# Kernel optimization log

Measured on AMD Instinct MI355X. Metric: run time of the kernel, lower is better.

## Reference

```python
import jax, jax.numpy as jnp
from jax import lax
import numpy as np

B, C, H, W = 4, 256, 64, 64
CQK = C // 8  # 32


def conv3x3(x, w, b):
    # x: [B,C_in,H,W], w: [C_out,C_in,3,3], b: [C_out]
    y = lax.conv_general_dilated(x, w, window_strides=(1, 1), padding='SAME',
                                 dimension_numbers=('NCHW', 'OIHW', 'NCHW'))
    return y + b[None, :, None, None]


def setup_inputs() -> dict:
    key = jax.random.key(0)
    ks = jax.random.split(key, 8)
    scale = 0.02
    return {
        'x': jax.random.normal(ks[0], (B, C, H, W), dtype=jnp.float32),
        'wq': jax.random.normal(ks[1], (CQK, C, 3, 3), dtype=jnp.float32) * scale,
        'bq': jax.random.normal(ks[2], (CQK,), dtype=jnp.float32) * scale,
        'wk': jax.random.normal(ks[3], (CQK, C, 3, 3), dtype=jnp.float32) * scale,
        'bk': jax.random.normal(ks[4], (CQK,), dtype=jnp.float32) * scale,
        'wv': jax.random.normal(ks[5], (C, C, 3, 3), dtype=jnp.float32) * scale,
        'bv': jax.random.normal(ks[6], (C,), dtype=jnp.float32) * scale,
        'gamma': jax.random.normal(ks[7], (1,), dtype=jnp.float32) * scale,
    }


def reference(x, wq, bq, wk, bk, wv, bv, gamma):
    b, c, h, w = x.shape
    n = h * w
    # Q: [B, N, C//8]  (permute(0,2,1) of the flattened conv output)
    q = conv3x3(x, wq, bq).reshape(b, -1, n).transpose(0, 2, 1)
    # K: [B, C//8, N]
    k = conv3x3(x, wk, bk).reshape(b, -1, n)
    # s: [B, N_q, N_k]
    s = jnp.einsum('bqd,bdk->bqk', q, k)
    # NOTE: original uses Softmax(dim=-2), i.e. over the QUERY axis
    attn_T = jax.nn.softmax(s, axis=-2)
    # V: [B, C, N]
    v = conv3x3(x, wv, bv).reshape(b, c, n)
    # o = bmm(V, attn_T): [B, C, N]
    o = jnp.einsum('bcq,bqk->bck', v, attn_T).reshape(b, c, h, w)
    return x + gamma * o
```

## Files before the change

### kernel.cpp

```cpp
#include <hip/hip_runtime.h>
#include <cstddef>

#define N_PIX 4096
#define HW 64
#define LOG2E 1.4426950408889634f
#define SHIFT2 28.8539008177793f

typedef __attribute__((ext_vector_type(8))) short bf16x8;
typedef __attribute__((ext_vector_type(4))) float f32x4;
typedef unsigned int u32;

static __device__ __forceinline__ unsigned short f2bf(float f) {
    union { float f; unsigned u; } v; v.f = f;
    unsigned r = v.u + 0x7fffu + ((v.u >> 16) & 1u);
    return (unsigned short)(r >> 16);
}
static __device__ __forceinline__ float bf2f(unsigned short s) {
    union { unsigned u; float f; } v; v.u = (unsigned)s << 16;
    return v.f;
}
static __device__ __forceinline__ unsigned pack_bf16_trunc(float lo, float hi) {
    union { float f; unsigned u; } a, b; a.f = hi; b.f = lo;
    return __builtin_amdgcn_perm(a.u, b.u, 0x07060302u);
}
static __device__ __forceinline__ void gll16(const void* g, void* l) {
    __builtin_amdgcn_global_load_lds(
        (const __attribute__((address_space(1))) u32*)g,
        (__attribute__((address_space(3))) u32*)l, 16, 0, 0);
}

__global__ __launch_bounds__(256) void prep_kernel(
    const float* __restrict__ x, unsigned short* __restrict__ xbf,
    const float* __restrict__ wq, const float* __restrict__ wk,
    const float* __restrict__ wv, unsigned short* __restrict__ wAll,
    unsigned short* __restrict__ zp)
{
    const int tid = threadIdx.x;
    if (blockIdx.z < 4) {
        __shared__ unsigned short Ts[64][72];
        const int px0 = blockIdx.x * 64, ci0 = blockIdx.y * 64, b = blockIdx.z;
        const float* xb = x + ((size_t)b * 256 + ci0) * N_PIX;

#pragma unroll
        for (int r = 0; r < 4; ++r) {
            int c = r * 16 + (tid >> 4);
            int p4 = (tid & 15) * 4;
            float4 v = *(const float4*)&xb[(size_t)c * N_PIX + px0 + p4];
            Ts[c][p4 + 0] = f2bf(v.x);
            Ts[c][p4 + 1] = f2bf(v.y);
            Ts[c][p4 + 2] = f2bf(v.z);
            Ts[c][p4 + 3] = f2bf(v.w);
        }
        __syncthreads();
#pragma unroll
        for (int r = 0; r < 2; ++r) {
            int id = tid * 2 + r;
            int p = id >> 3, c8 = (id & 7) * 8;
            ushort4 lo, hi;
            lo.x = Ts[c8 + 0][p]; lo.y = Ts[c8 + 1][p];
            lo.z = Ts[c8 + 2][p]; lo.w = Ts[c8 + 3][p];
            hi.x = Ts[c8 + 4][p]; hi.y = Ts[c8 + 5][p];
            hi.z = Ts[c8 + 6][p]; hi.w = Ts[c8 + 7][p];
            size_t off = ((size_t)b * N_PIX + px0 + p) * 256 + ci0 + c8;
            *(ushort4*)&xbf[off]     = lo;
            *(ushort4*)&xbf[off + 4] = hi;
        }
    } else {
        const int f = blockIdx.y * 64 + blockIdx.x;
#pragma unroll
        for (int base = 0; base < 2; ++base) {
            int gid = base * 65536 + f * 256 + tid;
            if (gid < 256) zp[gid] = 0;
            if (gid >= 72 * 320 * 4) continue;
            int part = gid & 3;
            int m = (gid >> 2) % 320;
            int kb = gid / 1280;
            int t = kb >> 3;
            int ci0 = (kb & 7) * 32 + part * 8;
            const float* src; int co; float sc = 1.f;
            if (m < 256)      { src = wv; co = m; }
            else if (m < 288) { src = wq; co = m - 256; sc = LOG2E; }
            else              { src = wk; co = m - 288; }
            ushort4 lo, hi;
            lo.x = f2bf(sc * src[((size_t)co * 256 + ci0 + 0) * 9 + t]);
            lo.y = f2bf(sc * src[((size_t)co * 256 + ci0 + 1) * 9 + t]);
            lo.z = f2bf(sc * src[((size_t)co * 256 + ci0 + 2) * 9 + t]);
            lo.w = f2bf(sc * src[((size_t)co * 256 + ci0 + 3) * 9 + t]);
            hi.x = f2bf(sc * src[((size_t)co * 256 + ci0 + 4) * 9 + t]);
            hi.y = f2bf(sc * src[((size_t)co * 256 + ci0 + 5) * 9 + t]);
            hi.z = f2bf(sc * src[((size_t)co * 256 + ci0 + 6) * 9 + t]);
            hi.w = f2bf(sc * src[((size_t)co * 256 + ci0 + 7) * 9 + t]);
            size_t off = ((size_t)kb * 320 + m) * 32 + part * 8;
            *(ushort4*)&wAll[off]     = lo;
            *(ushort4*)&wAll[off + 4] = hi;
        }
    }
}

__global__ __launch_bounds__(256, 2) void conv_gemm_v9(
    const unsigned short* __restrict__ xbf, const unsigned short* __restrict__ wAll,
    const float* __restrict__ bq, const float* __restrict__ bk,
    const float* __restrict__ bv, const unsigned short* __restrict__ zpage,
    unsigned short* __restrict__ vbf, unsigned short* __restrict__ qt,
    unsigned short* __restrict__ kt)
{
    __shared__ unsigned short Bl[3 * 7168];

    const int tid = threadIdx.x;
    const int w = tid >> 6, lane = tid & 63, quad = lane >> 4, l15 = lane & 15;
    const int y = blockIdx.x, rh = blockIdx.y, b = blockIdx.z;
    const int rg = w >> 1;
    const int pxh = w & 1;

    const unsigned short* xb = xbf + (size_t)b * N_PIX * 256;
    const unsigned short* aSrc = wAll + (size_t)rh * 160 * 32;

    auto stage = [&](int kb, int buf) {
        const int t_ = kb >> 3;
        const int ty = t_ / 3;
        const int dy = ty - 1, dx = t_ - ty * 3 - 1;
        const int gy = y + dy;
        const bool rowOK = ((unsigned)gy < 64u);
        const int ci0 = (kb & 7) * 32;
        const unsigned short* aS = aSrc + (size_t)kb * 10240;
        unsigned short* tile = &Bl[buf * 7168];
#pragma unroll
        for (int r = 0; r < 4; ++r) {
            const int c = r * 4 + w;
            if (r == 3 && w >= 2) continue;
            if (c < 10) {
                int o = c * 1024 + lane * 16;
                int u = o ^ (((o >> 7) & 7) << 4);
                gll16(aS + (u >> 1), tile + c * 512);
            } else {
                int o = (c - 10) * 1024 + lane * 16;
                int u = o ^ (((o >> 7) & 7) << 4);
                int px = u >> 6, k16 = (u >> 4) & 3;
                int gx = px + dx;
                const unsigned short* src =
                    (rowOK && (unsigned)gx < 64u)
                        ? xb + ((size_t)(gy * 64 + gx) * 256 + ci0 + k16 * 8)
                        : zpage;
                gll16(src, tile + 5120 + (c - 10) * 512);
            }
        }
    };

    f32x4 acc[5][2];
#pragma unroll
    for (int cb = 0; cb < 5; ++cb)
#pragma unroll
        for (int jb = 0; jb < 2; ++jb) acc[cb][jb] = (f32x4){0.f, 0.f, 0.f, 0.f};

    stage(0, 0);
    stage(1, 1);
    if (w < 2) asm volatile("s_waitcnt vmcnt(4)" ::: "memory");
    else       asm volatile("s_waitcnt vmcnt(3)" ::: "memory");
    __builtin_amdgcn_s_barrier();
    __builtin_amdgcn_sched_barrier(0);

#pragma unroll
    for (int kb = 0; kb < 72; ++kb) {
        const int buf = kb % 3;
        const int pb  = (kb + 2) % 3;
        const bool more2 = (kb + 2 < 72);
        const bool more1 = (kb + 1 < 72);
        if (more2) stage(kb + 2, pb);

        const int bb = buf * 7168;
        bf16x8 af[5], bfr[2];
#pragma unroll
        for (int cb = 0; cb < 5; ++cb) {
            int sr = rg * 80 + cb * 16 + l15;
            int u = sr * 64 + quad * 16;
            u ^= ((u >> 7) & 7) << 4;
            af[cb] = *(const bf16x8*)&Bl[bb + (u >> 1)];
        }
#pragma unroll
        for (int jb = 0; jb < 2; ++jb) {
            int px = pxh * 32 + jb * 16 + l15;
            int u = px * 64 + quad * 16;
            u ^= ((u >> 7) & 7) << 4;
            bfr[jb] = *(const bf16x8*)&Bl[bb + 5120 + (u >> 1)];
        }
        __builtin_amdgcn_s_setprio(1);
#pragma unroll
        for (int cb = 0; cb < 5; ++cb)
#pragma unroll
            for (int jb = 0; jb < 2; ++jb)
                acc[cb][jb] = __builtin_amdgcn_mfma_f32_16x16x32_bf16(
                    af[cb], bfr[jb], acc[cb][jb], 0, 0, 0);
        __builtin_amdgcn_s_setprio(0);

        if (more2) {
            if (w < 2) asm volatile("s_waitcnt vmcnt(4)" ::: "memory");
            else       asm volatile("s_waitcnt vmcnt(3)" ::: "memory");
        } else if (more1) {
            asm volatile("s_waitcnt vmcnt(0)" ::: "memory");
        }
        if (more1) {
            __builtin_amdgcn_s_barrier();
            __builtin_amdgcn_sched_barrier(0);
        }
    }

#pragma unroll
    for (int cb = 0; cb < 5; ++cb) {
        int cBase = rh * 160 + rg * 80 + cb * 16 + quad * 4;
#pragma unroll
        for (int r = 0; r < 4; ++r) {
            int c = cBase + r;
            if (c < 256) {
                float bias = bv[c];
#pragma unroll
                for (int jb = 0; jb < 2; ++jb) {
                    int px = y * 64 + pxh * 32 + jb * 16 + l15;
                    vbf[((size_t)b * 256 + c) * N_PIX + px] = f2bf(acc[cb][jb][r] + bias);
                }
            } else if (c < 288) {
                float bias = bq[c - 256] * LOG2E;
#pragma unroll
                for (int jb = 0; jb < 2; ++jb) {
                    int px = y * 64 + pxh * 32 + jb * 16 + l15;
                    qt[((size_t)b * N_PIX + px) * 32 + (c - 256)] = f2bf(acc[cb][jb][r] + bias);
                }
            } else {
                float bias = bk[c - 288];
#pragma unroll
                for (int jb = 0; jb < 2; ++jb) {
                    int px = y * 64 + pxh * 32 + jb * 16 + l15;
                    kt[((size_t)b * N_PIX + px) * 32 + (c - 288)] = f2bf(acc[cb][jb][r] + bias);
                }
            }
        }
    }
}

__global__ __launch_bounds__(256, 2) void fused_attn_mfma(
    const unsigned short* __restrict__ qt, const unsigned short* __restrict__ kt,
    const unsigned short* __restrict__ vbf,
    unsigned short* __restrict__ Abuf, float* __restrict__ lbuf, int iRange)
{
    const int tid  = threadIdx.x;
    const int w    = tid >> 6;
    const int lane = tid & 63;
    const int quad = lane >> 4;
    const int l15  = lane & 15;
    const int j0   = blockIdx.x * 128;
    const int b    = blockIdx.y;
    const int sp   = blockIdx.z;
    const int iBeg = sp * iRange;
    const int NI   = iRange / 64;

    const unsigned short* qtb = qt + (size_t)b * N_PIX * 32;
    const unsigned short* ktb = kt + (size_t)b * N_PIX * 32;
    const unsigned short* vb  = vbf + ((size_t)b * 256 + w * 64) * N_PIX;

    __shared__ unsigned Pfrag[2][4096];
    __shared__ unsigned short Vl[4][2][2048];
    __shared__ float lred[4][128];

    bf16x8 kf[8];
#pragma unroll
    for (int jb = 0; jb < 8; ++jb)
        kf[jb] = *(const bf16x8*)&ktb[((size_t)(j0 + jb * 16 + l15)) * 32 + quad * 8];

    f32x4 acc[4][8];
#pragma unroll
    for (int cb = 0; cb < 4; ++cb)
#pragma unroll
        for (int jb = 0; jb < 8; ++jb)
            acc[cb][jb] = (f32x4){0.f, 0.f, 0.f, 0.f};

    float lpart[8] = {0.f, 0.f, 0.f, 0.f, 0.f, 0.f, 0.f, 0.f};

    const int wFrag = w >> 1;
    const int wL    = ((w & 1) << 5) + ((quad >> 1) << 4) + l15;
    const int wEl2  = (quad & 1) << 1;

    auto stageV = [&](int c0, int vbuf) {
#pragma unroll
        for (int r = 0; r < 4; ++r) {
            int o = r * 1024 + lane * 16;
            int u = o ^ (((o >> 7) & 7) << 4);
            const unsigned short* src =
                vb + (size_t)(u >> 6) * N_PIX + c0 + ((u & 63) >> 1);
            gll16(src, &Vl[w][vbuf][r * 512]);
        }
    };
    auto readVa = [&](int vbuf, bf16x8 (&va)[4]) {
#pragma unroll
        for (int cb = 0; cb < 4; ++cb) {
            int o = (cb * 16 + l15) * 64 + quad * 16;
            int u = o ^ (((o >> 7) & 7) << 4);
            va[cb] = *(const bf16x8*)&Vl[w][vbuf][u >> 1];
        }
    };

    auto s_phase = [&](bf16x8 qa, int buf) {
#pragma unroll
        for (int jb = 0; jb < 8; ++jb) {
            f32x4 s = __builtin_amdgcn_mfma_f32_16x16x32_bf16(
                qa, kf[jb], (f32x4){-SHIFT2, -SHIFT2, -SHIFT2, -SHIFT2}, 0, 0, 0);
            float p0 = __builtin_amdgcn_exp2f(s[0]);
            float p1 = __builtin_amdgcn_exp2f(s[1]);
            float p2 = __builtin_amdgcn_exp2f(s[2]);
            float p3 = __builtin_amdgcn_exp2f(s[3]);
            lpart[jb] += (p0 + p1) + (p2 + p3);
            unsigned u0 = pack_bf16_trunc(p0, p1);
            unsigned u1 = pack_bf16_trunc(p2, p3);
            unsigned base = (((jb << 1) + wFrag) * 64 + wL) * 4 + wEl2;
            Pfrag[buf][base]     = u0;
            Pfrag[buf][base + 1] = u1;
        }
    };

    auto load_qa = [&](int i0) {
        return *(const bf16x8*)&qtb[((size_t)(i0 + w * 16 + l15)) * 32 + quad * 8];
    };

    stageV(iBeg, 0);
    stageV(iBeg + 32, 1);
    s_phase(load_qa(iBeg), 0);
    asm volatile("s_waitcnt lgkmcnt(0)" ::: "memory");
    __builtin_amdgcn_s_barrier();
    __builtin_amdgcn_sched_barrier(0);

    for (int n = 0; n < NI; ++n) {
        const bool hasN = (n + 1 < NI);
        const int inext = iBeg + (n + 1) * 64;
        bf16x8 qaN;
        if (hasN) qaN = load_qa(inext);

        bf16x8 pb[8], va[4];

#pragma unroll
        for (int jb = 0; jb < 8; ++jb)
            pb[jb] = *(const bf16x8*)&Pfrag[n & 1][((jb << 1) * 64 + lane) * 4];
        if (hasN) asm volatile("s_waitcnt vmcnt(5)" ::: "memory");
        else      asm volatile("s_waitcnt vmcnt(4)" ::: "memory");
        __builtin_amdgcn_sched_barrier(0);
        readVa(0, va);
        asm volatile("s_waitcnt lgkmcnt(0)" ::: "memory");
        __builtin_amdgcn_sched_barrier(0);
        if (hasN) stageV(inext, 0);
#pragma unroll
        for (int cb = 0; cb < 4; ++cb)
#pragma unroll
            for (int jb = 0; jb < 8; ++jb)
                acc[cb][jb] = __builtin_amdgcn_mfma_f32_16x16x32_bf16(
                    va[cb], pb[jb], acc[cb][jb], 0, 0, 0);

#pragma unroll
        for (int jb = 0; jb < 8; ++jb)
            pb[jb] = *(const bf16x8*)&Pfrag[n & 1][(((jb << 1) + 1) * 64 + lane) * 4];
        if (hasN) asm volatile("s_waitcnt vmcnt(5)" ::: "memory");
        else      asm volatile("s_waitcnt vmcnt(0)" ::: "memory");
        __builtin_amdgcn_sched_barrier(0);
        readVa(1, va);
        asm volatile("s_waitcnt lgkmcnt(0)" ::: "memory");
        __builtin_amdgcn_sched_barrier(0);
        if (hasN) stageV(inext + 32, 1);
#pragma unroll
        for (int cb = 0; cb < 4; ++cb)
#pragma unroll
            for (int jb = 0; jb < 8; ++jb)
                acc[cb][jb] = __builtin_amdgcn_mfma_f32_16x16x32_bf16(
                    va[cb], pb[jb], acc[cb][jb], 0, 0, 0);

        if (hasN) s_phase(qaN, (n + 1) & 1);
        asm volatile("s_waitcnt lgkmcnt(0)" ::: "memory");
        __builtin_amdgcn_s_barrier();
        __builtin_amdgcn_sched_barrier(0);
    }

#pragma unroll
    for (int jb = 0; jb < 8; ++jb) {
        float v = lpart[jb];
        v += __shfl_xor(v, 16, 64);
        v += __shfl_xor(v, 32, 64);
        lpart[jb] = v;
    }
    if (lane < 16) {
#pragma unroll
        for (int jb = 0; jb < 8; ++jb)
            lred[w][jb * 16 + l15] = lpart[jb];
    }
    __syncthreads();
    if (tid < 128) {
        float s = lred[0][tid] + lred[1][tid] + lred[2][tid] + lred[3][tid];
        lbuf[((size_t)sp * 4 + b) * N_PIX + j0 + tid] = s;
    }

    unsigned short* Ab = Abuf + ((size_t)sp * 4 + b) * 256 * N_PIX;
#pragma unroll
    for (int cb = 0; cb < 4; ++cb) {
        int c = w * 64 + cb * 16 + quad * 4;
#pragma unroll
        for (int jb = 0; jb < 8; ++jb) {
            int j = j0 + jb * 16 + l15;
#pragma unroll
            for (int r = 0; r < 4; ++r)
                Ab[(size_t)(c + r) * N_PIX + j] = f2bf(acc[cb][jb][r]);
        }
    }
}

__global__ __launch_bounds__(256) void combine_kernel(
    const unsigned short* __restrict__ A, const float* __restrict__ L,
    const float* __restrict__ x, const float* __restrict__ gamma,
    float* __restrict__ out, int split)
{
    const size_t CH = (size_t)4 * 256 * N_PIX;
    size_t flat = ((size_t)blockIdx.x * 256 + threadIdx.x) * 8;
    int j = (int)(flat & (N_PIX - 1));
    int b = (int)(flat >> 20);

    float a[8] = {0.f, 0.f, 0.f, 0.f, 0.f, 0.f, 0.f, 0.f};
    float l[8] = {0.f, 0.f, 0.f, 0.f, 0.f, 0.f, 0.f, 0.f};
    for (int s = 0; s < split; ++s) {
        ushort4 av0 = *(const ushort4*)&A[flat + (size_t)s * CH];
        ushort4 av1 = *(const ushort4*)&A[flat + (size_t)s * CH + 4];
        a[0] += bf2f(av0.x); a[1] += bf2f(av0.y); a[2] += bf2f(av0.z); a[3] += bf2f(av0.w);
        a[4] += bf2f(av1.x); a[5] += bf2f(av1.y); a[6] += bf2f(av1.z); a[7] += bf2f(av1.w);
        float4 l0 = *(const float4*)&L[((size_t)s * 4 + b) * N_PIX + j];
        float4 l1 = *(const float4*)&L[((size_t)s * 4 + b) * N_PIX + j + 4];
        l[0] += l0.x; l[1] += l0.y; l[2] += l0.z; l[3] += l0.w;
        l[4] += l1.x; l[5] += l1.y; l[6] += l1.z; l[7] += l1.w;
    }
    float g = gamma[0];
    float4 x0 = *(const float4*)&x[flat];
    float4 x1 = *(const float4*)&x[flat + 4];
    float4 o0, o1;
    o0.x = x0.x + g * a[0] / l[0];
    o0.y = x0.y + g * a[1] / l[1];
    o0.z = x0.z + g * a[2] / l[2];
    o0.w = x0.w + g * a[3] / l[3];
    o1.x = x1.x + g * a[4] / l[4];
    o1.y = x1.y + g * a[5] / l[5];
    o1.z = x1.z + g * a[6] / l[6];
    o1.w = x1.w + g * a[7] / l[7];
    *(float4*)&out[flat]     = o0;
    *(float4*)&out[flat + 4] = o1;
}

extern "C" void kernel_launch(void* const* d_in, const int* in_sizes, int n_in,
                              void* d_out, int out_size, void* d_ws, size_t ws_size,
                              hipStream_t stream)
{
    const float* x     = (const float*)d_in[0];
    const float* wq    = (const float*)d_in[1];
    const float* bq    = (const float*)d_in[2];
    const float* wk    = (const float*)d_in[3];
    const float* bk    = (const float*)d_in[4];
    const float* wv    = (const float*)d_in[5];
    const float* bv    = (const float*)d_in[6];
    const float* gamma = (const float*)d_in[7];
    float* out = (float*)d_out;

    const size_t szQTel  = (size_t)4 * N_PIX * 32;
    const size_t szVBFel = (size_t)4 * 256 * N_PIX;
    const size_t szXBFel = (size_t)4 * N_PIX * 256;
    const size_t szWel   = (size_t)72 * 320 * 32;
    const size_t fixedB  = (2 * szQTel + szVBFel + szXBFel + szWel + 256) * 2;

    int split = 4;
    while (split > 1) {
        size_t need = fixedB
                    + (size_t)split * 4 * 256 * N_PIX * 2
                    + (size_t)split * 4 * N_PIX * 4;
        if (need <= ws_size) break;
        split >>= 1;
    }

    unsigned short* Abuf = (unsigned short*)d_ws;
    float* lbuf = (float*)(Abuf + (size_t)split * 4 * 256 * N_PIX);
    unsigned short* qt    = (unsigned short*)(lbuf + (size_t)split * 4 * N_PIX);
    unsigned short* kt    = qt + szQTel;
    unsigned short* vbf   = kt + szQTel;
    unsigned short* xbf   = vbf + szVBFel;
    unsigned short* wAll  = xbf + szXBFel;
    unsigned short* zpage = wAll + szWel;

    prep_kernel<<<dim3(N_PIX / 64, 4, 5), 256, 0, stream>>>(
        x, xbf, wq, wk, wv, wAll, zpage);

    conv_gemm_v9<<<dim3(HW, 2, 4), 256, 0, stream>>>(
        xbf, wAll, bq, bk, bv, zpage, vbf, qt, kt);

    fused_attn_mfma<<<dim3(N_PIX / 128, 4, split), 256, 0, stream>>>(
        qt, kt, vbf, Abuf, lbuf, N_PIX / split);

    combine_kernel<<<dim3((4 * 256 * N_PIX) / (256 * 8)), 256, 0, stream>>>(
        Abuf, lbuf, x, gamma, out, split);
}
```

Baseline: 175.4 us.

## Single-buffer P fragments in LDS and raise occupancy to three blocks per CU

Removes the double-buffered Pfrag shared array, shrinking LDS use so a third workgroup can fit per CU, and raises launch_bounds to 3 blocks. To stay correct with one buffer, all P fragments are now read into registers up front, followed by an extra barrier before the next s_phase overwrites them. The cost is a second barrier per iteration and more live registers (pb0 and pb1) under a tighter register cap, which may cause spills.

```diff
diff --git a/kernel.cpp b/kernel.cpp
--- a/kernel.cpp
+++ b/kernel.cpp
@@ -236,7 +236,7 @@
     }
 }
 
-__global__ __launch_bounds__(256, 2) void fused_attn_mfma(
+__global__ __launch_bounds__(256, 3) void fused_attn_mfma(
     const unsigned short* __restrict__ qt, const unsigned short* __restrict__ kt,
     const unsigned short* __restrict__ vbf,
     unsigned short* __restrict__ Abuf, float* __restrict__ lbuf, int iRange)
@@ -256,7 +256,7 @@
     const unsigned short* ktb = kt + (size_t)b * N_PIX * 32;
     const unsigned short* vb  = vbf + ((size_t)b * 256 + w * 64) * N_PIX;
 
-    __shared__ unsigned Pfrag[2][4096];
+    __shared__ unsigned Pfrag[4096];
     __shared__ unsigned short Vl[4][2][2048];
     __shared__ float lred[4][128];
 
@@ -297,7 +297,7 @@
         }
     };
 
-    auto s_phase = [&](bf16x8 qa, int buf) {
+    auto s_phase = [&](bf16x8 qa) {
 #pragma unroll
         for (int jb = 0; jb < 8; ++jb) {
             f32x4 s = __builtin_amdgcn_mfma_f32_16x16x32_bf16(
@@ -310,8 +310,8 @@
             unsigned u0 = pack_bf16_trunc(p0, p1);
             unsigned u1 = pack_bf16_trunc(p2, p3);
             unsigned base = (((jb << 1) + wFrag) * 64 + wL) * 4 + wEl2;
-            Pfrag[buf][base]     = u0;
-            Pfrag[buf][base + 1] = u1;
+            Pfrag[base]     = u0;
+            Pfrag[base + 1] = u1;
         }
     };
 
@@ -321,7 +321,7 @@
 
     stageV(iBeg, 0);
     stageV(iBeg + 32, 1);
-    s_phase(load_qa(iBeg), 0);
+    s_phase(load_qa(iBeg));
     asm volatile("s_waitcnt lgkmcnt(0)" ::: "memory");
     __builtin_amdgcn_s_barrier();
     __builtin_amdgcn_sched_barrier(0);
@@ -332,11 +332,16 @@
         bf16x8 qaN;
         if (hasN) qaN = load_qa(inext);
 
-        bf16x8 pb[8], va[4];
-
-#pragma unroll
-        for (int jb = 0; jb < 8; ++jb)
-            pb[jb] = *(const bf16x8*)&Pfrag[n & 1][((jb << 1) * 64 + lane) * 4];
+        bf16x8 pb0[8], pb1[8], va[4];
+#pragma unroll
+        for (int jb = 0; jb < 8; ++jb) {
+            pb0[jb] = *(const bf16x8*)&Pfrag[((jb << 1) * 64 + lane) * 4];
+            pb1[jb] = *(const bf16x8*)&Pfrag[(((jb << 1) + 1) * 64 + lane) * 4];
+        }
+        asm volatile("s_waitcnt lgkmcnt(0)" ::: "memory");
+        __builtin_amdgcn_s_barrier();
+        __builtin_amdgcn_sched_barrier(0);
+
         if (hasN) asm volatile("s_waitcnt vmcnt(5)" ::: "memory");
         else      asm volatile("s_waitcnt vmcnt(4)" ::: "memory");
         __builtin_amdgcn_sched_barrier(0);
@@ -349,11 +354,8 @@
 #pragma unroll
             for (int jb = 0; jb < 8; ++jb)
                 acc[cb][jb] = __builtin_amdgcn_mfma_f32_16x16x32_bf16(
-                    va[cb], pb[jb], acc[cb][jb], 0, 0, 0);
-
-#pragma unroll
-        for (int jb = 0; jb < 8; ++jb)
-            pb[jb] = *(const bf16x8*)&Pfrag[n & 1][(((jb << 1) + 1) * 64 + lane) * 4];
+                    va[cb], pb0[jb], acc[cb][jb], 0, 0, 0);
+
         if (hasN) asm volatile("s_waitcnt vmcnt(5)" ::: "memory");
         else      asm volatile("s_waitcnt vmcnt(0)" ::: "memory");
         __builtin_amdgcn_sched_barrier(0);
@@ -366,9 +368,9 @@
 #pragma unroll
             for (int jb = 0; jb < 8; ++jb)
                 acc[cb][jb] = __builtin_amdgcn_mfma_f32_16x16x32_bf16(
-                    va[cb], pb[jb], acc[cb][jb], 0, 0, 0);
-
-        if (hasN) s_phase(qaN, (n + 1) & 1);
+                    va[cb], pb1[jb], acc[cb][jb], 0, 0, 0);
+
+        if (hasN) s_phase(qaN);
         asm volatile("s_waitcnt lgkmcnt(0)" ::: "memory");
         __builtin_amdgcn_s_barrier();
         __builtin_amdgcn_sched_barrier(0);
```

Measured after the change: 531.8 us. 3.03x slower.

## Give each wave private LDS double buffers in conv GEMM to drop barriers

Applied to the files above, without the earlier changes.

The conv GEMM now has each wave stage its own A (80 rows) and B (32 pixels) tiles into a private double-buffered LDS region, where before the block shared one triple-buffered tile. Every workgroup s_barrier in the K loop is removed and each wave syncs only through its own vmcnt/lgkmcnt waits. The cost is that data formerly shared is loaded more than once: waves with the same pixel half duplicate the B loads and waves with the same row group duplicate the A loads, which raises global/L2 traffic per block. LDS use is about the same (roughly 57KB against 43KB before).

```diff
diff --git a/kernel.cpp b/kernel.cpp
--- a/kernel.cpp
+++ b/kernel.cpp
@@ -97,14 +97,14 @@
     }
 }
 
-__global__ __launch_bounds__(256, 2) void conv_gemm_v9(
+__global__ __launch_bounds__(256, 2) void conv_gemm_v10(
     const unsigned short* __restrict__ xbf, const unsigned short* __restrict__ wAll,
     const float* __restrict__ bq, const float* __restrict__ bk,
     const float* __restrict__ bv, const unsigned short* __restrict__ zpage,
     unsigned short* __restrict__ vbf, unsigned short* __restrict__ qt,
     unsigned short* __restrict__ kt)
 {
-    __shared__ unsigned short Bl[3 * 7168];
+    __shared__ unsigned short Bl[4][2][3584];
 
     const int tid = threadIdx.x;
     const int w = tid >> 6, lane = tid & 63, quad = lane >> 4, l15 = lane & 15;
@@ -113,7 +113,7 @@
     const int pxh = w & 1;
 
     const unsigned short* xb = xbf + (size_t)b * N_PIX * 256;
-    const unsigned short* aSrc = wAll + (size_t)rh * 160 * 32;
+    const unsigned short* aSrcW = wAll + (size_t)(rh * 160 + rg * 80) * 32;
 
     auto stage = [&](int kb, int buf) {
         const int t_ = kb >> 3;
@@ -122,27 +122,26 @@
         const int gy = y + dy;
         const bool rowOK = ((unsigned)gy < 64u);
         const int ci0 = (kb & 7) * 32;
-        const unsigned short* aS = aSrc + (size_t)kb * 10240;
-        unsigned short* tile = &Bl[buf * 7168];
-#pragma unroll
-        for (int r = 0; r < 4; ++r) {
-            const int c = r * 4 + w;
-            if (r == 3 && w >= 2) continue;
-            if (c < 10) {
-                int o = c * 1024 + lane * 16;
-                int u = o ^ (((o >> 7) & 7) << 4);
-                gll16(aS + (u >> 1), tile + c * 512);
-            } else {
-                int o = (c - 10) * 1024 + lane * 16;
-                int u = o ^ (((o >> 7) & 7) << 4);
-                int px = u >> 6, k16 = (u >> 4) & 3;
-                int gx = px + dx;
-                const unsigned short* src =
-                    (rowOK && (unsigned)gx < 64u)
-                        ? xb + ((size_t)(gy * 64 + gx) * 256 + ci0 + k16 * 8)
-                        : zpage;
-                gll16(src, tile + 5120 + (c - 10) * 512);
-            }
+        const unsigned short* aS = aSrcW + (size_t)kb * 10240;
+        unsigned short* tile = &Bl[w][buf][0];
+#pragma unroll
+        for (int d = 0; d < 5; ++d) {
+            int o = d * 1024 + lane * 16;
+            int u = o ^ (((o >> 7) & 7) << 4);
+            gll16(aS + (u >> 1), tile + d * 512);
+        }
+#pragma unroll
+        for (int d = 0; d < 2; ++d) {
+            int o = d * 1024 + lane * 16;
+            int u = o ^ (((o >> 7) & 7) << 4);
+            int px = pxh * 32 + (u >> 6);
+            int k16 = (u >> 4) & 3;
+            int gx = px + dx;
+            const unsigned short* src =
+                (rowOK && (unsigned)gx < 64u)
+                    ? xb + ((size_t)(gy * 64 + gx) * 256 + ci0 + k16 * 8)
+                    : zpage;
+            gll16(src, tile + 2560 + d * 512);
         }
     };
 
@@ -154,35 +153,31 @@
 
     stage(0, 0);
     stage(1, 1);
-    if (w < 2) asm volatile("s_waitcnt vmcnt(4)" ::: "memory");
-    else       asm volatile("s_waitcnt vmcnt(3)" ::: "memory");
-    __builtin_amdgcn_s_barrier();
+    asm volatile("s_waitcnt vmcnt(7)" ::: "memory");
     __builtin_amdgcn_sched_barrier(0);
 
 #pragma unroll
     for (int kb = 0; kb < 72; ++kb) {
-        const int buf = kb % 3;
-        const int pb  = (kb + 2) % 3;
-        const bool more2 = (kb + 2 < 72);
-        const bool more1 = (kb + 1 < 72);
-        if (more2) stage(kb + 2, pb);
-
-        const int bb = buf * 7168;
+        const int buf = kb & 1;
+
         bf16x8 af[5], bfr[2];
 #pragma unroll
         for (int cb = 0; cb < 5; ++cb) {
-            int sr = rg * 80 + cb * 16 + l15;
-            int u = sr * 64 + quad * 16;
-            u ^= ((u >> 7) & 7) << 4;
-            af[cb] = *(const bf16x8*)&Bl[bb + (u >> 1)];
+            int o = (cb * 16 + l15) * 64 + quad * 16;
+            int u = o ^ (((o >> 7) & 7) << 4);
+            af[cb] = *(const bf16x8*)&Bl[w][buf][u >> 1];
         }
 #pragma unroll
         for (int jb = 0; jb < 2; ++jb) {
-            int px = pxh * 32 + jb * 16 + l15;
-            int u = px * 64 + quad * 16;
-            u ^= ((u >> 7) & 7) << 4;
-            bfr[jb] = *(const bf16x8*)&Bl[bb + 5120 + (u >> 1)];
-        }
+            int o = (jb * 16 + l15) * 64 + quad * 16;
+            int u = o ^ (((o >> 7) & 7) << 4);
+            bfr[jb] = *(const bf16x8*)&Bl[w][buf][2560 + (u >> 1)];
+        }
+        asm volatile("s_waitcnt lgkmcnt(0)" ::: "memory");
+        __builtin_amdgcn_sched_barrier(0);
+
+        if (kb + 2 < 72) stage(kb + 2, buf);
+
         __builtin_amdgcn_s_setprio(1);
 #pragma unroll
         for (int cb = 0; cb < 5; ++cb)
@@ -192,16 +187,12 @@
                     af[cb], bfr[jb], acc[cb][jb], 0, 0, 0);
         __builtin_amdgcn_s_setprio(0);
 
-        if (more2) {
-            if (w < 2) asm volatile("s_waitcnt vmcnt(4)" ::: "memory");
-            else       asm volatile("s_waitcnt vmcnt(3)" ::: "memory");
-        } else if (more1) {
+        if (kb + 2 < 72) {
+            asm volatile("s_waitcnt vmcnt(7)" ::: "memory");
+        } else if (kb + 1 < 72) {
             asm volatile("s_waitcnt vmcnt(0)" ::: "memory");
         }
-        if (more1) {
-            __builtin_amdgcn_s_barrier();
-            __builtin_amdgcn_sched_barrier(0);
-        }
+        __builtin_amdgcn_sched_barrier(0);
     }
 
 #pragma unroll
@@ -485,7 +476,7 @@
     prep_kernel<<<dim3(N_PIX / 64, 4, 5), 256, 0, stream>>>(
         x, xbf, wq, wk, wv, wAll, zpage);
 
-    conv_gemm_v9<<<dim3(HW, 2, 4), 256, 0, stream>>>(
+    conv_gemm_v10<<<dim3(HW, 2, 4), 256, 0, stream>>>(
         xbf, wAll, bq, bk, bv, zpage, vbf, qt, kt);
 
     fused_attn_mfma<<<dim3(N_PIX / 128, 4, split), 256, 0, stream>>>(
```

Result: slower. 179.3 us (+2.2%).
